# Performance work log

Measured on AMD Instinct MI355X. Metric: run time of the kernel, lower is better.

The kernel has to match this reference:

```python
import jax, jax.numpy as jnp
import numpy as np

B, N, C = 8, 4096, 512
H, DK, DV = 8, 64, 64


def _xnorm(x, gamma):
    # L2 norm over last dim, keepdim; scale by per-head gamma
    nrm = jnp.sqrt(jnp.sum(x * x, axis=-1, keepdims=True))
    return x * gamma / nrm


def setup_inputs() -> dict:
    key = jax.random.key(0)
    ks = jax.random.split(key, 9)
    inp = {
        "queries": jax.random.normal(ks[0], (B, N, C), dtype=jnp.float32),
        "keys": jax.random.normal(ks[1], (B, N, C), dtype=jnp.float32),
        "values": jax.random.normal(ks[2], (B, N, C), dtype=jnp.float32),
        # Linear weights stored torch-style [out, in]; init.normal_(std=0.001), bias=0
        "Wq": jax.random.normal(ks[3], (H * DK, C), dtype=jnp.float32) * 0.001,
        "bq": jnp.zeros((H * DK,), dtype=jnp.float32),
        "Wk": jax.random.normal(ks[4], (H * DK, C), dtype=jnp.float32) * 0.001,
        "bk": jnp.zeros((H * DK,), dtype=jnp.float32),
        "Wv": jax.random.normal(ks[5], (H * DV, C), dtype=jnp.float32) * 0.001,
        "bv": jnp.zeros((H * DV,), dtype=jnp.float32),
        "Wo": jax.random.normal(ks[6], (C, H * DV), dtype=jnp.float32) * 0.001,
        "bo": jnp.zeros((C,), dtype=jnp.float32),
        "gamma": jax.random.normal(ks[7], (1, H, 1, 1), dtype=jnp.float32),
    }
    return inp


def reference(queries, keys, values, Wq, bq, Wk, bk, Wv, bv, Wo, bo, gamma):
    bs, nq, _ = queries.shape
    nk = keys.shape[1]
    # projections -> [b, h, n, d]
    q = (queries @ Wq.T + bq).reshape(bs, nq, H, DK).transpose(0, 2, 1, 3)
    k = (keys @ Wk.T + bk).reshape(bs, nk, H, DK).transpose(0, 2, 1, 3)
    v = (values @ Wv.T + bv).reshape(bs, nk, H, DV).transpose(0, 2, 1, 3)
    # kv: [b, h, dk, dv]  (small intermediate)
    kv = jnp.einsum('bhnk,bhnv->bhkv', k, v)
    kv_n = _xnorm(kv, gamma)     # norm over dv
    q_n = _xnorm(q, gamma)       # norm over dk
    out = jnp.einsum('bhnk,bhkv->bhnv', q_n, kv_n)  # [b,h,nq,dv]
    out = out.transpose(0, 2, 1, 3).reshape(bs, nq, H * DV)
    return out @ Wo.T + bo
```

## Files before the change

kernel.cpp:

```cpp
#include <hip/hip_runtime.h>


typedef __attribute__((ext_vector_type(4))) float f32x4;
typedef __attribute__((ext_vector_type(8))) short s16x8;
typedef __attribute__((ext_vector_type(4))) unsigned short u16x4;
typedef __attribute__((ext_vector_type(4))) unsigned u32x4;

#define DEVFN __device__ __forceinline__

DEVFN unsigned short f2b(float f) {
  union { float f; unsigned u; } un; un.f = f;
  unsigned r = un.u + 0x7fffu + ((un.u >> 16) & 1u);
  return (unsigned short)(r >> 16);
}
DEVFN float b2f(unsigned short us) {
  union { unsigned u; float f; } un; un.u = ((unsigned)us) << 16;
  return un.f;
}
DEVFN unsigned pk2(float x0, float x1) {
  union { float f; unsigned u; } a, b;
  a.f = x0; b.f = x1;
  return __builtin_amdgcn_perm(b.u + 0x8000u, a.u + 0x8000u, 0x07060302u);
}
DEVFN void gl_lds16(const void* g, void* l) {
  __builtin_amdgcn_global_load_lds(
      (const __attribute__((address_space(1))) unsigned*)g,
      (__attribute__((address_space(3))) unsigned*)l, 16, 0, 0);
}

template <bool AF32, typename CT>
DEVFN void gemm256(const void* Ain, const unsigned short* Bt,
                   const float* bias, CT* C, bool qnorm, const float* gamma,
                   int bx, int by) {
  constexpr int NN = 512;
  __shared__ __align__(16) char LA[65536];
  __shared__ __align__(16) char LB[65536];
  const int tid = threadIdx.x, lane = tid & 63, wid = tid >> 6;
  const int r = lane & 15, g = lane >> 4;
  const int mw = wid >> 2;
  const int nw = wid & 3;

  const char* pa = LA + mw * 16384 + r * 128;
  const char* pb = LB + (nw >> 1) * 16384 + ((nw & 1) * 64 + r) * 128;
  const int sw0 = (g ^ (r & 7)) << 4;
  const int sw1 = ((4 + g) ^ (r & 7)) << 4;

  const char* BsS = (const char*)Bt + (long)(by * 256 + (tid >> 3)) * 1024 +
                    ((tid & 7) ^ ((tid >> 3) & 7)) * 16;
  char* BdS = LB + wid * 1024;

  const char* AsS = nullptr;
  const char* AfS = nullptr;
  char* AdS = LA + wid * 1024;
  int aw0 = 0, aw1 = 0;
  if constexpr (AF32) {
    AfS = (const char*)Ain + (long)(bx * 256 + (tid >> 2)) * 2048 +
          (tid & 3) * 64;
    const int rr = tid >> 2, s0 = (tid & 3) * 2;
    aw0 = rr * 128 + ((s0 ^ (rr & 7)) << 4);
    aw1 = rr * 128 + (((s0 + 1) ^ (rr & 7)) << 4);
  } else {
    AsS = (const char*)Ain + (long)(bx * 256 + (tid >> 3)) * 1024 +
          ((tid & 7) ^ ((tid >> 3) & 7)) * 16;
  }

  f32x4 acc[8][4] = {};
  s16x8 b0[4], b1[4];
  f32x4 rs0[4], rs1[4];

#define SB0 __builtin_amdgcn_sched_barrier(0);
#define BARR SB0 __builtin_amdgcn_s_barrier(); SB0
#define VMC(N) asm volatile("s_waitcnt vmcnt(" #N ")" ::: "memory");
#define LGK asm volatile("s_waitcnt lgkmcnt(0)" ::: "memory");

#define RA(dv, BUF, FOFF, SW)                                                  \
  _Pragma("unroll") for (int f = 0; f < 4; ++f)                                \
      dv[f] = *reinterpret_cast<const s16x8*>(pa + (BUF)*32768 + (FOFF) +      \
                                              f * 2048 + (SW));
#define RB(dv, BUF, SW)                                                        \
  _Pragma("unroll") for (int j = 0; j < 4; ++j)                                \
      dv[j] = *reinterpret_cast<const s16x8*>(pb + (BUF)*32768 + j * 2048 +    \
                                              (SW));
#define MM(av, bv, FB)                                                         \
  _Pragma("unroll") for (int f = 0; f < 4; ++f)                                \
      _Pragma("unroll") for (int j = 0; j < 4; ++j)                            \
      acc[(FB) + f][j] = __builtin_amdgcn_mfma_f32_16x16x32_bf16(              \
          av[f], bv[j], acc[(FB) + f][j], 0, 0, 0);

#define SGB(BUF, HALF, KT)                                                     \
  gl_lds16(BsS + ((HALF)*128) * 1024 + (KT)*128,                               \
           BdS + (BUF)*32768 + (HALF)*16384);                                  \
  gl_lds16(BsS + ((HALF)*128 + 64) * 1024 + (KT)*128,                          \
           BdS + (BUF)*32768 + (HALF)*16384 + 8192);
#define SGA(BUF, HALF, KT)                                                     \
  gl_lds16(AsS + ((HALF)*128) * 1024 + (KT)*128,                               \
           AdS + (BUF)*32768 + (HALF)*16384);                                  \
  gl_lds16(AsS + ((HALF)*128 + 64) * 1024 + (KT)*128,                          \
           AdS + (BUF)*32768 + (HALF)*16384 + 8192);
#define LDA(RS, HALF, KT)                                                      \
  _Pragma("unroll") for (int u = 0; u < 4; ++u)                                \
      RS[u] = *reinterpret_cast<const f32x4*>(AfS + (long)(HALF)*262144 +      \
                                              (KT)*256 + u * 16);
#define WRA(RS, BUF, HALF)                                                     \
  {                                                                            \
    unsigned w0 = pk2(RS[0][0], RS[0][1]), w1 = pk2(RS[0][2], RS[0][3]);       \
    unsigned w2 = pk2(RS[1][0], RS[1][1]), w3 = pk2(RS[1][2], RS[1][3]);       \
    unsigned w4 = pk2(RS[2][0], RS[2][1]), w5 = pk2(RS[2][2], RS[2][3]);       \
    unsigned w6 = pk2(RS[3][0], RS[3][1]), w7 = pk2(RS[3][2], RS[3][3]);       \
    *reinterpret_cast<u32x4*>(LA + (BUF)*32768 + (HALF)*16384 + aw0) =         \
        u32x4{w0, w1, w2, w3};                                                 \
    *reinterpret_cast<u32x4*>(LA + (BUF)*32768 + (HALF)*16384 + aw1) =         \
        u32x4{w4, w5, w6, w7};                                                 \
  }

  if constexpr (AF32) {
    LDA(rs0, 0, 0) LDA(rs1, 1, 0)
    WRA(rs0, 0, 0) WRA(rs1, 0, 1)
    SGB(0, 0, 0) SGB(0, 1, 0) SGB(1, 0, 1) SGB(1, 1, 1)
    asm volatile("s_waitcnt vmcnt(0) lgkmcnt(0)" ::: "memory");
    SB0
    LDA(rs0, 0, 1) LDA(rs1, 1, 1)
  } else {
    SGA(0, 0, 0) SGA(0, 1, 0)
    SGB(0, 0, 0) SGB(0, 1, 0) SGB(1, 0, 1) SGB(1, 1, 1)
    VMC(0)
  }
  BARR

#define ITER(KT0v, LASTv)                                                      \
  {                                                                    \
    s16x8 a[4];                                                                \
    RA(a, 0, 0, sw0) RB(b0, 0, sw0)                                            \
    if constexpr (AF32) { WRA(rs0, 1, 0) } else { SGA(1, 0, (KT0v) + 1) }      \
    BARR __builtin_amdgcn_s_setprio(1); MM(a, b0, 0)                           \
    __builtin_amdgcn_s_setprio(0);                                             \
    if constexpr (AF32) { LGK }                                                \
    BARR                                                                       \
  }                                                                            \
  {                                                                    \
    s16x8 a[4];                                                                \
    RA(a, 0, 0, sw1) RB(b1, 0, sw1)                                            \
    if constexpr (AF32) { WRA(rs1, 1, 1) } else { SGA(1, 1, (KT0v) + 1) }      \
    BARR __builtin_amdgcn_s_setprio(1); MM(a, b1, 0)                           \
    __builtin_amdgcn_s_setprio(0);                                             \
    if constexpr (AF32) { LGK }                                                \
    BARR                                                                       \
  }                                                                            \
  {                                                                    \
    s16x8 a[4];                                                                \
    RA(a, 0, 8192, sw0)                                                        \
    if (!(LASTv)) {                                                            \
      SGB(0, 0, (KT0v) + 2) SB0                                                \
      if constexpr (AF32) { LDA(rs0, 0, (KT0v) + 2) }                          \
    }                                                                          \
    BARR __builtin_amdgcn_s_setprio(1); MM(a, b0, 4)                           \
    __builtin_amdgcn_s_setprio(0); BARR                                        \
  }                                                                            \
  {                                                                    \
    s16x8 a[4];                                                                \
    RA(a, 0, 8192, sw1)                                                        \
    if (!(LASTv)) {                                                            \
      SGB(0, 1, (KT0v) + 2) SB0                                                \
      if constexpr (AF32) { LDA(rs1, 1, (KT0v) + 2) }                          \
      VMC(4)                                                                   \
    } else { VMC(0) }                                                          \
    BARR __builtin_amdgcn_s_setprio(1); MM(a, b1, 4)                           \
    __builtin_amdgcn_s_setprio(0); BARR                                        \
  }                                                                            \
  {                                                                    \
    s16x8 a[4];                                                                \
    RA(a, 1, 0, sw0) RB(b0, 1, sw0)                                            \
    if (!(LASTv)) {                                                            \
      if constexpr (AF32) { WRA(rs0, 0, 0) } else { SGA(0, 0, (KT0v) + 2) }    \
    }                                                                          \
    BARR __builtin_amdgcn_s_setprio(1); MM(a, b0, 0)                           \
    __builtin_amdgcn_s_setprio(0);                                             \
    if constexpr (AF32) { if (!(LASTv)) { LGK } }                              \
    BARR                                                                       \
  }                                                                            \
  {                                                                    \
    s16x8 a[4];                                                                \
    RA(a, 1, 0, sw1) RB(b1, 1, sw1)                                            \
    if (!(LASTv)) {                                                            \
      if constexpr (AF32) { WRA(rs1, 0, 1) } else { SGA(0, 1, (KT0v) + 2) }    \
    }                                                                          \
    BARR __builtin_amdgcn_s_setprio(1); MM(a, b1, 0)                           \
    __builtin_amdgcn_s_setprio(0);                                             \
    if constexpr (AF32) { if (!(LASTv)) { LGK } }                              \
    BARR                                                                       \
  }                                                                            \
  {                                                                    \
    s16x8 a[4];                                                                \
    RA(a, 1, 8192, sw0)                                                        \
    if (!(LASTv)) {                                                            \
      SGB(1, 0, (KT0v) + 3) SB0                                                \
      if constexpr (AF32) { LDA(rs0, 0, (KT0v) + 3) }                          \
    }                                                                          \
    BARR __builtin_amdgcn_s_setprio(1); MM(a, b0, 4)                           \
    __builtin_amdgcn_s_setprio(0); BARR                                        \
  }                                                                            \
  {                                                                    \
    s16x8 a[4];                                                                \
    RA(a, 1, 8192, sw1)                                                        \
    if (!(LASTv)) {                                                            \
      SGB(1, 1, (KT0v) + 3) SB0                                                \
      if constexpr (AF32) { LDA(rs1, 1, (KT0v) + 3) }                          \
      VMC(4)                                                                   \
    }                                                                          \
    BARR __builtin_amdgcn_s_setprio(1); MM(a, b1, 4)                           \
    __builtin_amdgcn_s_setprio(0); BARR                                        \
  }

  ITER(0, 0)
  ITER(2, 0)
  ITER(4, 0)
  ITER(6, 1)

#undef ITER
#undef RA
#undef RB
#undef MM
#undef SGB
#undef SGA
#undef LDA
#undef WRA
#undef SB0
#undef BARR
#undef VMC
#undef LGK

  const int crow0 = bx * 256 + mw * 128 + g * 4;
  const int ccol0 = by * 256 + nw * 64 + r;
#pragma unroll
  for (int j = 0; j < 4; ++j) {
    float bv = bias[ccol0 + j * 16];
#pragma unroll
    for (int f = 0; f < 8; ++f)
#pragma unroll
      for (int ii = 0; ii < 4; ++ii) acc[f][j][ii] += bv;
  }
  if (qnorm) {
    const float gam = gamma[by * 4 + nw];
#pragma unroll
    for (int f = 0; f < 8; ++f)
#pragma unroll
      for (int ii = 0; ii < 4; ++ii) {
        float s = 0.f;
#pragma unroll
        for (int j = 0; j < 4; ++j) s += acc[f][j][ii] * acc[f][j][ii];
        s += __shfl_xor(s, 1);
        s += __shfl_xor(s, 2);
        s += __shfl_xor(s, 4);
        s += __shfl_xor(s, 8);
        float sc = gam / sqrtf(s);
#pragma unroll
        for (int j = 0; j < 4; ++j) acc[f][j][ii] *= sc;
      }
  }
#pragma unroll
  for (int f = 0; f < 8; ++f)
#pragma unroll
    for (int j = 0; j < 4; ++j)
#pragma unroll
      for (int ii = 0; ii < 4; ++ii) {
        long row = crow0 + f * 16 + ii;
        int col = ccol0 + j * 16;
        if constexpr (sizeof(CT) == 2)
          C[row * NN + col] = f2b(acc[f][j][ii]);
        else
          C[row * NN + col] = acc[f][j][ii];
      }
}

__global__ __launch_bounds__(512, 1)
void proj_qkv(const float* __restrict__ Aq, const float* __restrict__ Ak,
              const float* __restrict__ Av, const unsigned short* __restrict__ Bq,
              const unsigned short* __restrict__ Bk, const unsigned short* __restrict__ Bv,
              const float* __restrict__ bq, const float* __restrict__ bk,
              const float* __restrict__ bv, unsigned short* __restrict__ Cq,
              unsigned short* __restrict__ Ck, unsigned short* __restrict__ Cv,
              const float* __restrict__ gamma) {
  const int z = blockIdx.y;
  const float* A = z == 0 ? Aq : (z == 1 ? Ak : Av);
  const unsigned short* B = z == 0 ? Bq : (z == 1 ? Bk : Bv);
  const float* bias = z == 0 ? bq : (z == 1 ? bk : bv);
  unsigned short* C = z == 0 ? Cq : (z == 1 ? Ck : Cv);
  const int bid = blockIdx.x;
  const int s = (bid & 7) * 32 + (bid >> 3);
  gemm256<true, unsigned short>(A, B, bias, C, z == 0, gamma, s >> 1, s & 1);
}

__global__ __launch_bounds__(512, 1)
void gemm_final(const unsigned short* __restrict__ q, const unsigned short* __restrict__ Mt,
                const float* __restrict__ bo, float* __restrict__ out) {
  const int zb = blockIdx.y;
  const int bid = blockIdx.x;
  const int s = (bid & 7) * 4 + (bid >> 3);
  gemm256<false, float>(q + (long)zb * 2097152, Mt + (long)zb * 262144, bo,
                        out + (long)zb * 2097152, false, nullptr, s >> 1,
                        s & 1);
}

#define NCHUNK 16
__global__ __launch_bounds__(256, 2)
void kv_partial(const unsigned short* __restrict__ kq,
                const unsigned short* __restrict__ vq,
                float* __restrict__ part) {
  const int tid = threadIdx.x;
  const int chunk = blockIdx.x;
  const int bh = blockIdx.y;
  const int b = bh >> 3, h = bh & 7;
  __shared__ float ks[32][64];
  __shared__ float vs[32][64];
  const int dk0 = (tid & 15) * 4;
  const int dv0 = (tid >> 4) * 4;
  float acc[4][4] = {};
  const long nbase = (long)b * 4096 + chunk * 256;

  for (int sub = 0; sub < 8; ++sub) {
    long n0 = nbase + sub * 32;
#pragma unroll
    for (int i = 0; i < 2; ++i) {
      int e = i * 256 + tid;
      int row = e >> 4, c4 = e & 15;
      long gofs = (n0 + row) * 512 + h * 64 + c4 * 4;
      u16x4 kk = *reinterpret_cast<const u16x4*>(kq + gofs);
      u16x4 vv = *reinterpret_cast<const u16x4*>(vq + gofs);
      f32x4 kf = {b2f(kk[0]), b2f(kk[1]), b2f(kk[2]), b2f(kk[3])};
      f32x4 vf = {b2f(vv[0]), b2f(vv[1]), b2f(vv[2]), b2f(vv[3])};
      *reinterpret_cast<f32x4*>(&ks[row][c4 * 4]) = kf;
      *reinterpret_cast<f32x4*>(&vs[row][c4 * 4]) = vf;
    }
    __syncthreads();
#pragma unroll 4
    for (int n = 0; n < 32; ++n) {
      f32x4 kk = *reinterpret_cast<const f32x4*>(&ks[n][dk0]);
      f32x4 vv = *reinterpret_cast<const f32x4*>(&vs[n][dv0]);
#pragma unroll
      for (int a = 0; a < 4; ++a)
#pragma unroll
        for (int c = 0; c < 4; ++c)
          acc[a][c] += kk[a] * vv[c];
    }
    __syncthreads();
  }
  float* pg = part + ((long)chunk * 64 + bh) * 4096;
#pragma unroll
  for (int a = 0; a < 4; ++a) {
    f32x4 o = {acc[a][0], acc[a][1], acc[a][2], acc[a][3]};
    *reinterpret_cast<f32x4*>(pg + (dk0 + a) * 64 + dv0) = o;
  }
}

__global__ __launch_bounds__(256)
void kv_normN(const float* __restrict__ part, const float* __restrict__ gamma,
              unsigned short* __restrict__ kvn) {
  const int bh = blockIdx.x, h = bh & 7;
  const int tid = threadIdx.x;
  __shared__ float kvs[4096];
  __shared__ float scale[64];
#pragma unroll
  for (int i = 0; i < 4; ++i) {
    int e4 = i * 256 + tid;
    const float* p = part + (long)bh * 4096 + e4 * 4;
    f32x4 s = {0.f, 0.f, 0.f, 0.f};
#pragma unroll
    for (int c = 0; c < NCHUNK; ++c) {
      f32x4 v = *reinterpret_cast<const f32x4*>(p + (long)c * 64 * 4096);
      s += v;
    }
    *reinterpret_cast<f32x4*>(kvs + e4 * 4) = s;
  }
  __syncthreads();
  if (tid < 64) {
    float s = 0.f;
    for (int dv = 0; dv < 64; ++dv) { float x = kvs[tid * 64 + dv]; s += x * x; }
    scale[tid] = gamma[h] / sqrtf(s);
  }
  __syncthreads();
#pragma unroll
  for (int i = 0; i < 4; ++i) {
    int e4 = i * 256 + tid;
    float sc = scale[e4 >> 4];
    f32x4 v = *reinterpret_cast<const f32x4*>(kvs + e4 * 4);
    u16x4 o = {f2b(v[0] * sc), f2b(v[1] * sc), f2b(v[2] * sc), f2b(v[3] * sc)};
    *reinterpret_cast<u16x4*>(kvn + (long)bh * 4096 + e4 * 4) = o;
  }
}

__global__ __launch_bounds__(64)
void mt_kernel(const unsigned short* __restrict__ Wo_b,
               const unsigned short* __restrict__ kvn,
               unsigned short* __restrict__ Mt) {
  const int bid = blockIdx.x;
  const int bh = bid >> 2, seg = bid & 3;
  const int b = bh >> 3, h = bh & 7;
  const int lane = threadIdx.x;
  const int r = lane & 15, g = lane >> 4;
  f32x4 acc[8][4] = {};
  s16x8 bf[2][4];
#pragma unroll
  for (int ks = 0; ks < 2; ++ks)
#pragma unroll
    for (int j = 0; j < 4; ++j)
      bf[ks][j] = *reinterpret_cast<const s16x8*>(
          kvn + (long)bh * 4096 + (j * 16 + r) * 64 + ks * 32 + g * 8);
#pragma unroll
  for (int ks = 0; ks < 2; ++ks)
#pragma unroll
    for (int i = 0; i < 8; ++i) {
      s16x8 af = *reinterpret_cast<const s16x8*>(
          Wo_b + (long)(seg * 128 + i * 16 + r) * 512 + h * 64 + ks * 32 + g * 8);
#pragma unroll
      for (int j = 0; j < 4; ++j)
        acc[i][j] = __builtin_amdgcn_mfma_f32_16x16x32_bf16(af, bf[ks][j], acc[i][j], 0, 0, 0);
    }
#pragma unroll
  for (int i = 0; i < 8; ++i)
#pragma unroll
    for (int j = 0; j < 4; ++j)
#pragma unroll
      for (int ii = 0; ii < 4; ++ii) {
        int c = seg * 128 + i * 16 + g * 4 + ii;
        int dk = j * 16 + r;
        Mt[(long)b * 262144 + (long)c * 512 + h * 64 + dk] = f2b(acc[i][j][ii]);
      }
}

__global__ void cast4(const float* __restrict__ a0, const float* __restrict__ a1,
                      const float* __restrict__ a2, const float* __restrict__ a3,
                      unsigned short* __restrict__ o0, unsigned short* __restrict__ o1,
                      unsigned short* __restrict__ o2, unsigned short* __restrict__ o3) {
  const int y = blockIdx.y;
  const float* in = y == 0 ? a0 : (y == 1 ? a1 : (y == 2 ? a2 : a3));
  unsigned short* out = y == 0 ? o0 : (y == 1 ? o1 : (y == 2 ? o2 : o3));
  int i = blockIdx.x * 256 + threadIdx.x;
  f32x4 v = reinterpret_cast<const f32x4*>(in)[i];
  reinterpret_cast<u16x4*>(out)[i] = u16x4{f2b(v[0]), f2b(v[1]), f2b(v[2]), f2b(v[3])};
}

extern "C" void kernel_launch(void* const* d_in, const int* in_sizes, int n_in,
                              void* d_out, int out_size, void* d_ws, size_t ws_size,
                              hipStream_t stream) {
  const float* queries = (const float*)d_in[0];
  const float* keys    = (const float*)d_in[1];
  const float* values  = (const float*)d_in[2];
  const float* Wq = (const float*)d_in[3];
  const float* bq = (const float*)d_in[4];
  const float* Wk = (const float*)d_in[5];
  const float* bk = (const float*)d_in[6];
  const float* Wv = (const float*)d_in[7];
  const float* bv = (const float*)d_in[8];
  const float* Wo = (const float*)d_in[9];
  const float* bo = (const float*)d_in[10];
  const float* gamma = (const float*)d_in[11];

  unsigned short* Wq_b = (unsigned short*)d_ws;
  unsigned short* Wk_b = Wq_b + 262144;
  unsigned short* Wv_b = Wk_b + 262144;
  unsigned short* Wo_b = Wv_b + 262144;
  unsigned short* q_b  = Wo_b + 262144;
  unsigned short* kvn  = q_b + 16777216;
  float* part = (float*)(kvn + 262144);
  unsigned short* Mt = (unsigned short*)part;
  unsigned short* k_b = (unsigned short*)d_out;
  unsigned short* v_b = k_b + 16777216;
  float* out = (float*)d_out;

  cast4<<<dim3(256, 4), 256, 0, stream>>>(Wq, Wk, Wv, Wo, Wq_b, Wk_b, Wv_b, Wo_b);

  proj_qkv<<<dim3(256, 3), 512, 0, stream>>>(
      queries, keys, values, Wq_b, Wk_b, Wv_b, bq, bk, bv, q_b, k_b, v_b, gamma);

  kv_partial<<<dim3(NCHUNK, 64), 256, 0, stream>>>(k_b, v_b, part);
  kv_normN<<<64, 256, 0, stream>>>(part, gamma, kvn);
  mt_kernel<<<256, 64, 0, stream>>>(Wo_b, kvn, Mt);

  gemm_final<<<dim3(32, 8), 512, 0, stream>>>(q_b, Mt, bo, out);
}
```

Before: 178.5 us.

## Merge GEMM pipeline phases to halve barriers and roll the k-loop

Fuses pairs of the eight per-iteration MFMA phases into four larger phases. Each phase now issues both sw0/sw1 fragment reads and both global or LDS staging operations, then runs the two MFMA groups back to back under raised priority. This removes the barrier before each MFMA block and the explicit lgkmcnt waits, cutting synchronization and letting more loads overlap compute. The main k-loop becomes a non-unrolled loop with the final iteration peeled. The trade-off is higher register pressure from holding two A-fragment sets, and the correctness of the LDS write-after-read ordering now rests on the remaining barriers.

```diff
diff --git a/kernel.cpp b/kernel.cpp
--- a/kernel.cpp
+++ b/kernel.cpp
@@ -71,7 +71,8 @@
 #define SB0 __builtin_amdgcn_sched_barrier(0);
 #define BARR SB0 __builtin_amdgcn_s_barrier(); SB0
 #define VMC(N) asm volatile("s_waitcnt vmcnt(" #N ")" ::: "memory");
-#define LGK asm volatile("s_waitcnt lgkmcnt(0)" ::: "memory");
+#define SETP1 __builtin_amdgcn_s_setprio(1);
+#define SETP0 __builtin_amdgcn_s_setprio(0);
 
 #define RA(dv, BUF, FOFF, SW)                                                  \
   _Pragma("unroll") for (int f = 0; f < 4; ++f)                                \
@@ -127,96 +128,57 @@
   }
   BARR
 
-#define ITER(KT0v, LASTv)                                                      \
-  {                                                                    \
-    s16x8 a[4];                                                                \
-    RA(a, 0, 0, sw0) RB(b0, 0, sw0)                                            \
-    if constexpr (AF32) { WRA(rs0, 1, 0) } else { SGA(1, 0, (KT0v) + 1) }      \
-    BARR __builtin_amdgcn_s_setprio(1); MM(a, b0, 0)                           \
-    __builtin_amdgcn_s_setprio(0);                                             \
-    if constexpr (AF32) { LGK }                                                \
+#define ITERP(KT0v, LASTv)                                                     \
+  {                                                                \
+    s16x8 a0[4], a1[4];                                                        \
+    RA(a0, 0, 0, sw0) RB(b0, 0, sw0)                                           \
+    RA(a1, 0, 0, sw1) RB(b1, 0, sw1)                                           \
+    if constexpr (AF32) { WRA(rs0, 1, 0) WRA(rs1, 1, 1) }                      \
+    else { SGA(1, 0, (KT0v) + 1) SGA(1, 1, (KT0v) + 1) }                       \
+    SETP1 MM(a0, b0, 0) MM(a1, b1, 0) SETP0                                    \
     BARR                                                                       \
   }                                                                            \
-  {                                                                    \
-    s16x8 a[4];                                                                \
-    RA(a, 0, 0, sw1) RB(b1, 0, sw1)                                            \
-    if constexpr (AF32) { WRA(rs1, 1, 1) } else { SGA(1, 1, (KT0v) + 1) }      \
-    BARR __builtin_amdgcn_s_setprio(1); MM(a, b1, 0)                           \
-    __builtin_amdgcn_s_setprio(0);                                             \
-    if constexpr (AF32) { LGK }                                                \
+  {                                                                \
+    s16x8 a0[4], a1[4];                                                        \
+    RA(a0, 0, 8192, sw0) RA(a1, 0, 8192, sw1)                                  \
+    if (!(LASTv)) {                                                            \
+      SGB(0, 0, (KT0v) + 2) SGB(0, 1, (KT0v) + 2)                              \
+      if constexpr (AF32) { LDA(rs0, 0, (KT0v) + 2) LDA(rs1, 1, (KT0v) + 2) }  \
+    }                                                                          \
+    SETP1 MM(a0, b0, 4) MM(a1, b1, 4) SETP0                                    \
+    if constexpr (!AF32) { if (LASTv) { VMC(0) } else { VMC(4) } }             \
     BARR                                                                       \
   }                                                                            \
-  {                                                                    \
-    s16x8 a[4];                                                                \
-    RA(a, 0, 8192, sw0)                                                        \
+  {                                                                \
+    s16x8 a0[4], a1[4];                                                        \
+    RA(a0, 1, 0, sw0) RB(b0, 1, sw0)                                           \
+    RA(a1, 1, 0, sw1) RB(b1, 1, sw1)                                           \
     if (!(LASTv)) {                                                            \
-      SGB(0, 0, (KT0v) + 2) SB0                                                \
-      if constexpr (AF32) { LDA(rs0, 0, (KT0v) + 2) }                          \
+      if constexpr (AF32) { WRA(rs0, 0, 0) WRA(rs1, 0, 1) }                    \
+      else { SGA(0, 0, (KT0v) + 2) SGA(0, 1, (KT0v) + 2) }                     \
     }                                                                          \
-    BARR __builtin_amdgcn_s_setprio(1); MM(a, b0, 4)                           \
-    __builtin_amdgcn_s_setprio(0); BARR                                        \
-  }                                                                            \
-  {                                                                    \
-    s16x8 a[4];                                                                \
-    RA(a, 0, 8192, sw1)                                                        \
-    if (!(LASTv)) {                                                            \
-      SGB(0, 1, (KT0v) + 2) SB0                                                \
-      if constexpr (AF32) { LDA(rs1, 1, (KT0v) + 2) }                          \
-      VMC(4)                                                                   \
-    } else { VMC(0) }                                                          \
-    BARR __builtin_amdgcn_s_setprio(1); MM(a, b1, 4)                           \
-    __builtin_amdgcn_s_setprio(0); BARR                                        \
-  }                                                                            \
-  {                                                                    \
-    s16x8 a[4];                                                                \
-    RA(a, 1, 0, sw0) RB(b0, 1, sw0)                                            \
-    if (!(LASTv)) {                                                            \
-      if constexpr (AF32) { WRA(rs0, 0, 0) } else { SGA(0, 0, (KT0v) + 2) }    \
-    }                                                                          \
-    BARR __builtin_amdgcn_s_setprio(1); MM(a, b0, 0)                           \
-    __builtin_amdgcn_s_setprio(0);                                             \
-    if constexpr (AF32) { if (!(LASTv)) { LGK } }                              \
+    SETP1 MM(a0, b0, 0) MM(a1, b1, 0) SETP0                                    \
     BARR                                                                       \
   }                                                                            \
-  {                                                                    \
-    s16x8 a[4];                                                                \
-    RA(a, 1, 0, sw1) RB(b1, 1, sw1)                                            \
+  {                                                                \
+    s16x8 a0[4], a1[4];                                                        \
+    RA(a0, 1, 8192, sw0) RA(a1, 1, 8192, sw1)                                  \
     if (!(LASTv)) {                                                            \
-      if constexpr (AF32) { WRA(rs1, 0, 1) } else { SGA(0, 1, (KT0v) + 2) }    \
+      SGB(1, 0, (KT0v) + 3) SGB(1, 1, (KT0v) + 3)                              \
+      if constexpr (AF32) { LDA(rs0, 0, (KT0v) + 3) LDA(rs1, 1, (KT0v) + 3) }  \
     }                                                                          \
-    BARR __builtin_amdgcn_s_setprio(1); MM(a, b1, 0)                           \
-    __builtin_amdgcn_s_setprio(0);                                             \
-    if constexpr (AF32) { if (!(LASTv)) { LGK } }                              \
+    SETP1 MM(a0, b0, 4) MM(a1, b1, 4) SETP0                                    \
+    if constexpr (!AF32) { if (!(LASTv)) { VMC(4) } }                          \
     BARR                                                                       \
-  }                                                                            \
-  {                                                                    \
-    s16x8 a[4];                                                                \
-    RA(a, 1, 8192, sw0)                                                        \
-    if (!(LASTv)) {                                                            \
-      SGB(1, 0, (KT0v) + 3) SB0                                                \
-      if constexpr (AF32) { LDA(rs0, 0, (KT0v) + 3) }                          \
-    }                                                                          \
-    BARR __builtin_amdgcn_s_setprio(1); MM(a, b0, 4)                           \
-    __builtin_amdgcn_s_setprio(0); BARR                                        \
-  }                                                                            \
-  {                                                                    \
-    s16x8 a[4];                                                                \
-    RA(a, 1, 8192, sw1)                                                        \
-    if (!(LASTv)) {                                                            \
-      SGB(1, 1, (KT0v) + 3) SB0                                                \
-      if constexpr (AF32) { LDA(rs1, 1, (KT0v) + 3) }                          \
-      VMC(4)                                                                   \
-    }                                                                          \
-    BARR __builtin_amdgcn_s_setprio(1); MM(a, b1, 4)                           \
-    __builtin_amdgcn_s_setprio(0); BARR                                        \
-  }
-
-  ITER(0, 0)
-  ITER(2, 0)
-  ITER(4, 0)
-  ITER(6, 1)
-
-#undef ITER
+  }
+
+#pragma unroll 1
+  for (int kt0 = 0; kt0 < 6; kt0 += 2) {
+    ITERP(kt0, 0)
+  }
+  ITERP(6, 1)
+
+#undef ITERP
 #undef RA
 #undef RB
 #undef MM
@@ -227,7 +189,8 @@
 #undef SB0
 #undef BARR
 #undef VMC
-#undef LGK
+#undef SETP1
+#undef SETP0
 
   const int crow0 = bx * 256 + mw * 128 + g * 4;
   const int ccol0 = by * 256 + nw * 64 + r;
```

New measurement: 176.5 us. Within noise of the previous version (-1.1%).
